# Kernel tuning notes

Measured on AMD Instinct MI355X. Metric: run time of the kernel, lower is better.

The kernel has to match this reference:

```python
import jax, jax.numpy as jnp
import numpy as np
from jax import lax

NH = 8        # num_heads
NWIN = 7      # n_win
TOPK = 4


def setup_inputs() -> dict:
    key = jax.random.key(0)
    ks = jax.random.split(key, 7)
    B, C, H, W = 16, 256, 56, 56
    x = jax.random.normal(ks[0], (B, C, H, W), dtype=jnp.float32)
    s = 1.0 / np.sqrt(C)
    qkv_w = jax.random.normal(ks[1], (3 * C, C), dtype=jnp.float32) * s   # 1x1 conv
    qkv_b = jnp.zeros((3 * C,), dtype=jnp.float32)
    lepe_w = jax.random.normal(ks[2], (C, 1, 5, 5), dtype=jnp.float32) * 0.2  # depthwise 5x5
    lepe_b = jnp.zeros((C,), dtype=jnp.float32)
    out_w = jax.random.normal(ks[3], (C, C), dtype=jnp.float32) * s       # 1x1 conv
    out_b = jnp.zeros((C,), dtype=jnp.float32)
    return {"x": x, "qkv_w": qkv_w, "qkv_b": qkv_b, "lepe_w": lepe_w,
            "lepe_b": lepe_b, "out_w": out_w, "out_b": out_b}


def reference(x, qkv_w, qkv_b, lepe_w, lepe_b, out_w, out_b):
    B, C, H, W = x.shape
    rs0, rs1 = max(1, H // NWIN), max(1, W // NWIN)   # region size (H,W assumed divisible)
    rh, rw = H // rs0, W // rs1
    nreg, reg = rh * rw, rs0 * rs1
    hd = C // NH
    scale = C ** (-0.5)

    # qkv projection (1x1 conv == channel matmul)
    qkv = jnp.einsum('bchw,oc->bohw', x, qkv_w) + qkv_b[None, :, None, None]
    q, k, v = jnp.split(qkv, 3, axis=1)

    # region-level pooling (avg_pool over exact region blocks)
    def pool(t):
        return t.reshape(B, C, rh, rs0, rw, rs1).mean(axis=(3, 5))  # (B,C,rh,rw)
    q_r = pool(q).reshape(B, C, nreg).transpose(0, 2, 1)   # (B, nreg, C)
    k_r = pool(k).reshape(B, C, nreg)                      # (B, C, nreg)
    a_r = q_r @ k_r                                        # (B, nreg, nreg)
    _, idx = lax.top_k(a_r, TOPK)                          # (B, nreg, topk)

    # grid -> sequence: (B,C,H,W) -> (B,NH,nreg,reg,hd)
    def g2s(t):
        t = t.reshape(B, NH, hd, rh, rs0, rw, rs1)
        t = t.transpose(0, 1, 3, 5, 4, 6, 2)  # b,m,h,w,p,q,d
        return t.reshape(B, NH, nreg, reg, hd)

    qs, ks_, vs = g2s(q), g2s(k), g2s(v)

    # gather top-k kv regions per query region
    idx_h = jnp.broadcast_to(idx[:, None], (B, NH, nreg, TOPK))
    gidx = idx_h.reshape(B, NH, nreg * TOPK)[..., None, None]   # (B,NH,nreg*topk,1,1)
    kg = jnp.take_along_axis(ks_, gidx, axis=2).reshape(B, NH, nreg, TOPK * reg, hd)
    vg = jnp.take_along_axis(vs, gidx, axis=2).reshape(B, NH, nreg, TOPK * reg, hd)

    attn = jax.nn.softmax(jnp.einsum('bhnrd,bhnkd->bhnrk', qs * scale, kg), axis=-1)
    out = jnp.einsum('bhnrk,bhnkd->bhnrd', attn, vg)  # (B,NH,nreg,reg,hd)

    # sequence -> grid
    out = out.reshape(B, NH, rh, rw, rs0, rs1, hd)
    out = out.transpose(0, 1, 6, 2, 4, 3, 5).reshape(B, C, H, W)

    # LePE: depthwise 5x5 conv on v
    lepe = lax.conv_general_dilated(v, lepe_w, (1, 1), 'SAME',
                                    feature_group_count=C,
                                    dimension_numbers=('NCHW', 'OIHW', 'NCHW'))
    lepe = lepe + lepe_b[None, :, None, None]

    out = out + lepe
    out = jnp.einsum('bchw,oc->bohw', out, out_w) + out_b[None, :, None, None]
    return out
```

## Files before the change

### kernel.cpp

```cpp
#include <hip/hip_runtime.h>

typedef __attribute__((ext_vector_type(8))) short short8;
typedef __attribute__((ext_vector_type(4))) float f32x4;
typedef unsigned int uint;

constexpr int Bn    = 16;
constexpr int Cn    = 256;
constexpr int Hn    = 56;
constexpr int Wn    = 56;
constexpr int HWn   = Hn * Wn;
constexpr int NPn   = 3200;
constexpr int NHn   = 8;
constexpr int RWn   = 7;
constexpr int NREGn = 49;
constexpr int TOPKn = 4;
constexpr float QKSf = 0.0625f * 1.44269504088896f;

__device__ __forceinline__ float b2f(ushort u) { return __builtin_bit_cast(float, (uint)u << 16); }
__device__ __forceinline__ float b2fl(uint u) { return __builtin_bit_cast(float, u << 16); }
__device__ __forceinline__ float b2fh(uint u) { return __builtin_bit_cast(float, u & 0xffff0000u); }
__device__ __forceinline__ ushort f2b(float f) {
    uint u = __builtin_bit_cast(uint, f);
    u = (u + 0x7fffu + ((u >> 16) & 1u)) >> 16;
    return (ushort)u;
}

typedef __attribute__((address_space(3))) uint lds_u32_t;
typedef __attribute__((address_space(1))) const uint glb_u32_t;
__device__ __forceinline__ void gl_lds16(const ushort* g, ushort* l) {
    __builtin_amdgcn_global_load_lds((glb_u32_t*)g, (lds_u32_t*)l, 16, 0, 0);
}

__global__ __launch_bounds__(256)
void fill_pads(uint* __restrict__ xt, uint* __restrict__ yt)
{
    const int gid = blockIdx.x * 256 + threadIdx.x;
    const int arr = gid >> 17;
    const int e   = gid & 131071;
    const int b   = e >> 13;
    const int off = e & 8191;
    uint* base = arr ? yt : xt;
    base[(size_t)b * (NPn * Cn / 2) + (HWn * Cn / 2) + off] = 0u;
}

__global__ __launch_bounds__(256)
void convert_w(const float* __restrict__ qw, const float* __restrict__ ow,
               ushort* __restrict__ wq, ushort* __restrict__ wo)
{
    const int e = (blockIdx.x * 256 + threadIdx.x) * 4;
    if (e < 196608) {
        const float4 v = *(const float4*)(qw + e);
        *(ushort4*)(wq + e) = make_ushort4(f2b(v.x), f2b(v.y), f2b(v.z), f2b(v.w));
    } else {
        const int e2 = e - 196608;
        const float4 v = *(const float4*)(ow + e2);
        *(ushort4*)(wo + e2) = make_ushort4(f2b(v.x), f2b(v.y), f2b(v.z), f2b(v.w));
    }
}

__global__ __launch_bounds__(256)
void convert_x(const float* __restrict__ x, ushort* __restrict__ xt)
{
    __shared__ float tile[64][65];
    const int p0 = blockIdx.x * 64, c0 = blockIdx.y * 64, b = blockIdx.z;
    const int tid = threadIdx.x;
    #pragma unroll
    for (int it = 0; it < 4; ++it) {
        const int slot = it * 256 + tid;
        const int c = slot >> 4, p4 = (slot & 15) << 2;
        const float4 v = *(const float4*)(x + ((size_t)b * Cn + c0 + c) * HWn + p0 + p4);
        tile[c][p4 + 0] = v.x; tile[c][p4 + 1] = v.y;
        tile[c][p4 + 2] = v.z; tile[c][p4 + 3] = v.w;
    }
    __syncthreads();
    #pragma unroll
    for (int it = 0; it < 4; ++it) {
        const int slot = it * 256 + tid;
        const int p = slot >> 4, c4 = (slot & 15) << 2;
        ushort4 w4 = make_ushort4(f2b(tile[c4 + 0][p]), f2b(tile[c4 + 1][p]),
                                  f2b(tile[c4 + 2][p]), f2b(tile[c4 + 3][p]));
        *(ushort4*)(xt + ((size_t)b * NPn + p0 + p) * Cn + c0 + c4) = w4;
    }
}

__global__ __launch_bounds__(256)
void pool_x(const float* __restrict__ x, float* __restrict__ xr)
{
    const int gid = blockIdx.x * 256 + threadIdx.x;
    if (gid >= Bn * Cn * NREGn) return;
    const int r = gid % NREGn;
    const int t = gid / NREGn;
    const int c = t % Cn, b = t / Cn;
    const float* plane = x + ((size_t)b * Cn + c) * HWn + (r / RWn) * 8 * Wn + (r % RWn) * 8;
    float s = 0.f;
    #pragma unroll
    for (int p = 0; p < 8; ++p) {
        const float4 a  = *(const float4*)(plane + p * Wn);
        const float4 b4 = *(const float4*)(plane + p * Wn + 4);
        s += a.x + a.y + a.z + a.w + b4.x + b4.y + b4.z + b4.w;
    }
    xr[gid] = s * (1.0f / 64.0f);
}

__global__ __launch_bounds__(256)
void qkr_gemm(const float* __restrict__ qw, const float* __restrict__ qb,
              const float* __restrict__ xr, float* __restrict__ qr,
              float* __restrict__ kr)
{
    const int gid = blockIdx.x * 256 + threadIdx.x;
    const int j = gid % NREGn;
    const int t = gid / NREGn;
    const int m = t & 511;
    const int b = t >> 9;
    const float* wr = qw + (size_t)m * Cn;
    const float* xb = xr + (size_t)b * Cn * NREGn + j;
    float s = 0.f;
    #pragma unroll 8
    for (int c = 0; c < Cn; ++c)
        s = fmaf(wr[c], xb[c * NREGn], s);
    s += qb[m];
    if (m < Cn) qr[((size_t)b * Cn + m) * NREGn + j] = s;
    else        kr[((size_t)b * Cn + (m - Cn)) * NREGn + j] = s;
}

__global__ __launch_bounds__(256)
void routing(const float* __restrict__ qr, const float* __restrict__ kr,
             int* __restrict__ idxo)
{
    const int ig = blockIdx.x, b = blockIdx.y;
    __shared__ float ksh[Cn][NREGn];
    __shared__ float qsh[Cn][7];
    __shared__ float ar[7][NREGn];
    const float* qb = qr + (size_t)b * Cn * NREGn;
    const float* kb = kr + (size_t)b * Cn * NREGn;
    for (int rr = 0; rr < NREGn; ++rr)
        ksh[threadIdx.x][rr] = kb[threadIdx.x * NREGn + rr];
    for (int e = threadIdx.x; e < Cn * 7; e += 256)
        qsh[e / 7][e % 7] = qb[(e / 7) * NREGn + ig * 7 + (e % 7)];
    __syncthreads();
    for (int e = threadIdx.x; e < 7 * NREGn; e += 256) {
        const int il = e / NREGn, j = e % NREGn;
        float s = 0.f;
        for (int c = 0; c < Cn; ++c)
            s = fmaf(qsh[c][il], ksh[c][j], s);
        ar[il][j] = s;
    }
    __syncthreads();
    if (threadIdx.x < 7) {
        const int il = threadIdx.x;
        float bv0 = -3.0e38f, bv1 = -3.0e38f, bv2 = -3.0e38f, bv3 = -3.0e38f;
        int bi0 = 0, bi1 = 0, bi2 = 0, bi3 = 0;
        for (int j = 0; j < NREGn; ++j) {
            const float v = ar[il][j];
            if (v > bv3) {
                if (v > bv0)      { bv3=bv2; bi3=bi2; bv2=bv1; bi2=bi1; bv1=bv0; bi1=bi0; bv0=v; bi0=j; }
                else if (v > bv1) { bv3=bv2; bi3=bi2; bv2=bv1; bi2=bi1; bv1=v; bi1=j; }
                else if (v > bv2) { bv3=bv2; bi3=bi2; bv2=v; bi2=j; }
                else              { bv3=v; bi3=j; }
            }
        }
        int* o = idxo + ((size_t)b * NREGn + ig * 7 + il) * TOPKn;
        o[0] = bi0; o[1] = bi1; o[2] = bi2; o[3] = bi3;
    }
}

template<int MODE>
__global__ __launch_bounds__(256)
void gemm_mfma(const ushort* __restrict__ Wb, const float* __restrict__ bias,
               const ushort* __restrict__ Bt,
               ushort* __restrict__ oq, ushort* __restrict__ ok,
               ushort* __restrict__ ovt, float* __restrict__ of)
{
    constexpr int K = Cn;
    int bb, bx, by;
    {
        const int flat = blockIdx.x;
        if (MODE == 0) {
            const int sw = (flat & 7) * 300 + (flat >> 3);
            bb = sw / 150; const int r2 = sw % 150; bx = r2 / 6; by = r2 % 6;
        } else {
            const int sw = (flat & 7) * 100 + (flat >> 3);
            bb = sw / 50;  const int r2 = sw % 50;  bx = r2 / 2; by = r2 % 2;
        }
    }
    const int n0 = bx * 128;
    const int m0 = by * 128;
    __shared__ ushort As[128 * 32];
    __shared__ ushort Bs[128 * 32];
    const int tid = threadIdx.x;
    const int wid = tid >> 6, lane = tid & 63;
    const int wm = wid >> 1, wn = wid & 1;
    const ushort* Bb = Bt + (size_t)bb * NPn * K;

    f32x4 acc[4][4];
    #pragma unroll
    for (int i = 0; i < 4; ++i)
        #pragma unroll
        for (int j = 0; j < 4; ++j)
            acc[i][j] = (f32x4){0.f, 0.f, 0.f, 0.f};

    const int cA = wid * 64 + lane;
    const int rowA = cA >> 2, koffA = (cA & 3) << 3;

    for (int k0 = 0; k0 < K; k0 += 32) {
        gl_lds16(Wb + (size_t)(m0 + rowA) * K + k0 + koffA, As + wid * 512);
        gl_lds16(Wb + (size_t)(m0 + rowA + 64) * K + k0 + koffA, As + 2048 + wid * 512);
        gl_lds16(Bb + (size_t)(n0 + rowA) * K + k0 + koffA, Bs + wid * 512);
        gl_lds16(Bb + (size_t)(n0 + rowA + 64) * K + k0 + koffA, Bs + 2048 + wid * 512);
        __syncthreads();
        short8 a[4], b[4];
        #pragma unroll
        for (int i = 0; i < 4; ++i)
            a[i] = *(const short8*)(As + (wm * 64 + i * 16 + (lane & 15)) * 32 + ((lane >> 4) << 3));
        #pragma unroll
        for (int j = 0; j < 4; ++j)
            b[j] = *(const short8*)(Bs + (wn * 64 + j * 16 + (lane & 15)) * 32 + ((lane >> 4) << 3));
        #pragma unroll
        for (int i = 0; i < 4; ++i)
            #pragma unroll
            for (int j = 0; j < 4; ++j)
                acc[i][j] = __builtin_amdgcn_mfma_f32_16x16x32_bf16(a[i], b[j], acc[i][j], 0, 0, 0);
        __syncthreads();
    }

    if (MODE == 0) {
        #pragma unroll
        for (int i = 0; i < 4; ++i) {
            const int m_base = m0 + wm * 64 + i * 16;
            const int which = m_base >> 8;
            const int hh = (m_base >> 5) & 7;
            const int db = (m_base & 31) + ((lane >> 4) << 2);
            const float4 b4 = *(const float4*)(bias + m_base + ((lane >> 4) << 2));
            #pragma unroll
            for (int j = 0; j < 4; ++j) {
                const int n = n0 + wn * 64 + j * 16 + (lane & 15);
                if (n < HWn) {
                    const int py = n / 56, px = n % 56;
                    const int rr = (py >> 3) * 7 + (px >> 3);
                    const int ss = ((py & 7) << 3) + (px & 7);
                    if (which == 0) {
                        ushort4 w4 = make_ushort4(
                            f2b((acc[i][j][0] + b4.x) * QKSf), f2b((acc[i][j][1] + b4.y) * QKSf),
                            f2b((acc[i][j][2] + b4.z) * QKSf), f2b((acc[i][j][3] + b4.w) * QKSf));
                        *(ushort4*)(oq + (((size_t)bb * NHn + hh) * HWn + rr * 64 + ss) * 32 + db) = w4;
                    } else if (which == 1) {
                        ushort4 w4 = make_ushort4(f2b(acc[i][j][0] + b4.x), f2b(acc[i][j][1] + b4.y),
                                                  f2b(acc[i][j][2] + b4.z), f2b(acc[i][j][3] + b4.w));
                        *(ushort4*)(ok + (((size_t)bb * NHn + hh) * HWn + rr * 64 + ss) * 32 + db) = w4;
                    } else {
                        const size_t vtb = ((size_t)(bb * NHn + hh) * 32 + db) * HWn + rr * 64 + ss;
                        ovt[vtb + 0 * HWn] = f2b(acc[i][j][0] + b4.x);
                        ovt[vtb + 1 * HWn] = f2b(acc[i][j][1] + b4.y);
                        ovt[vtb + 2 * HWn] = f2b(acc[i][j][2] + b4.z);
                        ovt[vtb + 3 * HWn] = f2b(acc[i][j][3] + b4.w);
                    }
                }
            }
        }
    } else {
        #pragma unroll
        for (int i = 0; i < 4; ++i) {
            const int mb = m0 + wm * 64 + i * 16 + ((lane >> 4) << 2);
            const float4 b4 = *(const float4*)(bias + mb);
            #pragma unroll
            for (int j = 0; j < 4; ++j) {
                const int n = n0 + wn * 64 + j * 16 + (lane & 15);
                if (n < HWn) {
                    const int rr = n >> 6, ss = n & 63;
                    const int py = (rr / 7) * 8 + (ss >> 3);
                    const int px = (rr % 7) * 8 + (ss & 7);
                    float* od = of + ((size_t)bb * Cn + mb) * HWn + py * 56 + px;
                    od[0 * HWn] = acc[i][j][0] + b4.x;
                    od[1 * HWn] = acc[i][j][1] + b4.y;
                    od[2 * HWn] = acc[i][j][2] + b4.z;
                    od[3 * HWn] = acc[i][j][3] + b4.w;
                }
            }
        }
    }
}

__global__ __launch_bounds__(256)
void lepe(const ushort* __restrict__ vt, const float* __restrict__ lw,
          const float* __restrict__ lb, ushort* __restrict__ lbuf)
{
    const int gid = blockIdx.x * 256 + threadIdx.x;
    const int plane = gid / 392;
    const int within = gid - plane * 392;
    const int row = within / 7;
    const int sx  = within - row * 7;
    const int px0 = sx * 8;
    const int c = plane & 255;
    const ushort* vp = vt + (size_t)plane * HWn;
    const float* wc = lw + c * 25;

    float wreg[25];
    #pragma unroll
    for (int i = 0; i < 25; ++i) wreg[i] = wc[i];

    float acc[8];
    const float bias = lb[c];
    #pragma unroll
    for (int j = 0; j < 8; ++j) acc[j] = bias;

    #pragma unroll
    for (int kh = 0; kh < 5; ++kh) {
        const int iy = row + kh - 2;
        if (iy < 0 || iy >= Hn) continue;
        const int ry = iy >> 3, il = iy & 7;
        const ushort* rp = vp + (ry * 7 + sx) * 64 + il * 8;
        const uint  a = *(const uint*)(rp - 64 + 6);
        const uint4 M = *(const uint4*)(rp);
        const uint  e = *(const uint*)(rp + 64);
        float w[12];
        w[0]  = (px0 >= 2)      ? b2fl(a)   : 0.f;
        w[1]  = (px0 >= 1)      ? b2fh(a)   : 0.f;
        w[2]  = b2fl(M.x); w[3]  = b2fh(M.x);
        w[4]  = b2fl(M.y); w[5]  = b2fh(M.y);
        w[6]  = b2fl(M.z); w[7]  = b2fh(M.z);
        w[8]  = b2fl(M.w); w[9]  = b2fh(M.w);
        w[10] = (px0 + 8 < Wn)  ? b2fl(e)   : 0.f;
        w[11] = (px0 + 9 < Wn)  ? b2fh(e)   : 0.f;
        #pragma unroll
        for (int kw = 0; kw < 5; ++kw) {
            const float ww = wreg[kh * 5 + kw];
            #pragma unroll
            for (int j = 0; j < 8; ++j)
                acc[j] = fmaf(w[j + kw], ww, acc[j]);
        }
    }
    ushort* op = lbuf + (size_t)plane * HWn + ((row >> 3) * 7 + sx) * 64 + (row & 7) * 8;
    *(ushort4*)(op)     = make_ushort4(f2b(acc[0]), f2b(acc[1]), f2b(acc[2]), f2b(acc[3]));
    *(ushort4*)(op + 4) = make_ushort4(f2b(acc[4]), f2b(acc[5]), f2b(acc[6]), f2b(acc[7]));
}

__global__ __launch_bounds__(256, 2)
void attention3(const ushort* __restrict__ qs, const ushort* __restrict__ ks,
                const ushort* __restrict__ vt, const int* __restrict__ idxp,
                const ushort* __restrict__ lep, ushort* __restrict__ yt)
{
    const int flat = blockIdx.x;
    const int sw = (flat & 7) * 196 + (flat >> 3);
    const int b = sw / 98;
    const int rem = sw % 98;
    const int r = rem % 49;
    const int wid = threadIdx.x >> 6, lane = threadIdx.x & 63;
    const int h = (rem / 49) * 4 + wid;
    const int col = lane & 15, g = lane >> 4;
    __shared__ ushort plds_all[4][4096];
    ushort* pw = plds_all[wid];

    const size_t hb = ((size_t)b * NHn + h) * HWn;
    const size_t vtb = (size_t)(b * NHn + h) * 32;

    short8 qf[4];
    #pragma unroll
    for (int qt = 0; qt < 4; ++qt)
        qf[qt] = *(const short8*)(qs + (hb + (size_t)r * 64 + qt * 16 + col) * 32 + g * 8);

    f32x4 o[4][2];
    #pragma unroll
    for (int qt = 0; qt < 4; ++qt) {
        o[qt][0] = (f32x4){0.f, 0.f, 0.f, 0.f};
        o[qt][1] = (f32x4){0.f, 0.f, 0.f, 0.f};
    }
    float mrow[4] = {-3.0e38f, -3.0e38f, -3.0e38f, -3.0e38f};
    float lrow[4] = {0.f, 0.f, 0.f, 0.f};

    const int* ip = idxp + ((size_t)b * NREGn + r) * TOPKn;

    for (int t = 0; t < TOPKn; ++t) {
        const int rr = ip[t];
        short8 kf[4];
        #pragma unroll
        for (int kt = 0; kt < 4; ++kt)
            kf[kt] = *(const short8*)(ks + (hb + (size_t)rr * 64 + kt * 16 + col) * 32 + g * 8);
        short8 vf[2][2];
        #pragma unroll
        for (int dt = 0; dt < 2; ++dt)
            #pragma unroll
            for (int kc = 0; kc < 2; ++kc)
                vf[dt][kc] = *(const short8*)(vt + (vtb + dt * 16 + col) * HWn
                                              + (size_t)rr * 64 + kc * 32 + g * 8);

        f32x4 s[4][4];
        #pragma unroll
        for (int qt = 0; qt < 4; ++qt)
            #pragma unroll
            for (int kt = 0; kt < 4; ++kt)
                s[qt][kt] = __builtin_amdgcn_mfma_f32_16x16x32_bf16(
                    kf[kt], qf[qt], (f32x4){0.f, 0.f, 0.f, 0.f}, 0, 0, 0);

        #pragma unroll
        for (int qt = 0; qt < 4; ++qt) {
            float mx = s[qt][0][0];
            #pragma unroll
            for (int kt = 0; kt < 4; ++kt)
                #pragma unroll
                for (int e = 0; e < 4; ++e)
                    mx = fmaxf(mx, s[qt][kt][e]);
            mx = fmaxf(mx, __shfl_xor(mx, 16));
            mx = fmaxf(mx, __shfl_xor(mx, 32));
            const float mnew = fmaxf(mrow[qt], mx);
            const float corr = exp2f(mrow[qt] - mnew);
            mrow[qt] = mnew;
            float ps = 0.f;
            #pragma unroll
            for (int kt = 0; kt < 4; ++kt)
                #pragma unroll
                for (int e = 0; e < 4; ++e) {
                    const float p = exp2f(s[qt][kt][e] - mnew);
                    s[qt][kt][e] = p; ps += p;
                }
            ps += __shfl_xor(ps, 16);
            ps += __shfl_xor(ps, 32);
            lrow[qt] = lrow[qt] * corr + ps;
            const int qrow = qt * 16 + col;
            const int swz = (qrow & 7) << 4;
            #pragma unroll
            for (int kt = 0; kt < 4; ++kt) {
                ushort4 pk = make_ushort4(f2b(s[qt][kt][0]), f2b(s[qt][kt][1]),
                                          f2b(s[qt][kt][2]), f2b(s[qt][kt][3]));
                const int byt = (qrow * 128 + kt * 32 + g * 8) ^ swz;
                *(ushort4*)((char*)pw + byt) = pk;
            }
            #pragma unroll
            for (int reg = 0; reg < 4; ++reg) {
                const float cr = __shfl(corr, g * 4 + reg);
                o[qt][0][reg] *= cr;
                o[qt][1][reg] *= cr;
            }
        }
        #pragma unroll
        for (int kc = 0; kc < 2; ++kc)
            #pragma unroll
            for (int qt = 0; qt < 4; ++qt) {
                const int qrow = qt * 16 + col;
                const int byt = (qrow * 128 + kc * 64 + g * 16) ^ ((qrow & 7) << 4);
                const short8 pf = *(const short8*)((const char*)pw + byt);
                o[qt][0] = __builtin_amdgcn_mfma_f32_16x16x32_bf16(pf, vf[0][kc], o[qt][0], 0, 0, 0);
                o[qt][1] = __builtin_amdgcn_mfma_f32_16x16x32_bf16(pf, vf[1][kc], o[qt][1], 0, 0, 0);
            }
    }

    #pragma unroll
    for (int qt = 0; qt < 4; ++qt) {
        const float linv = 1.0f / lrow[qt];
        #pragma unroll
        for (int reg = 0; reg < 4; ++reg) {
            const float li = __shfl(linv, g * 4 + reg);
            const int row = qt * 16 + g * 4 + reg;
            const int swz = ((row >> 1) & 3) << 4;
            #pragma unroll
            for (int dt = 0; dt < 2; ++dt) {
                const int byt = (row * 64 + (dt * 16 + col) * 2) ^ swz;
                *(ushort*)((char*)pw + byt) = f2b(o[qt][dt][reg] * li);
            }
        }
    }
    const ushort* lp = lep + ((size_t)b * Cn + h * 32) * HWn + (size_t)r * 64 + lane;
    ushort* yp = yt + ((size_t)b * NPn + (size_t)r * 64 + lane) * Cn + h * 32;
    const int swl = ((lane >> 1) & 3) << 4;
    #pragma unroll
    for (int c4 = 0; c4 < 8; ++c4) {
        const int byt = (lane * 64 + c4 * 8) ^ swl;
        const ushort4 ov = *(const ushort4*)((const char*)pw + byt);
        ushort4 w4 = make_ushort4(
            f2b(b2f(ov.x) + b2f(lp[(size_t)(c4 * 4 + 0) * HWn])),
            f2b(b2f(ov.y) + b2f(lp[(size_t)(c4 * 4 + 1) * HWn])),
            f2b(b2f(ov.z) + b2f(lp[(size_t)(c4 * 4 + 2) * HWn])),
            f2b(b2f(ov.w) + b2f(lp[(size_t)(c4 * 4 + 3) * HWn])));
        *(ushort4*)(yp + c4 * 4) = w4;
    }
}

extern "C" void kernel_launch(void* const* d_in, const int* in_sizes, int n_in,
                              void* d_out, int out_size, void* d_ws, size_t ws_size,
                              hipStream_t stream)
{
    const float* x      = (const float*)d_in[0];
    const float* qkv_w  = (const float*)d_in[1];
    const float* qkv_b  = (const float*)d_in[2];
    const float* lepe_w = (const float*)d_in[3];
    const float* lepe_b = (const float*)d_in[4];
    const float* out_w  = (const float*)d_in[5];
    const float* out_b  = (const float*)d_in[6];
    float* out = (float*)d_out;

    char* ws = (char*)d_ws;
    ushort* XT = (ushort*)(ws);
    ushort* YT = (ushort*)(ws + 26214400);
    ushort* QS = (ushort*)(ws + 52428800);
    ushort* KS = (ushort*)(ws + 78118912);
    ushort* VT = (ushort*)(ws + 103809024);
    ushort* LB = (ushort*)(ws + 129499136);
    ushort* WQ = (ushort*)(ws + 155189248);
    ushort* WO = (ushort*)(ws + 155582464);
    float*  XR = (float*)(ws + 155713536);
    float*  QR = (float*)(ws + 156516352);
    float*  KR = (float*)(ws + 157319168);
    int*   IDX = (int*)(ws + 158121984);

    fill_pads<<<1024, 256, 0, stream>>>((uint*)XT, (uint*)YT);
    convert_w<<<256, 256, 0, stream>>>(qkv_w, out_w, WQ, WO);
    convert_x<<<dim3(49, 4, 16), 256, 0, stream>>>(x, XT);
    pool_x<<<(Bn * Cn * NREGn + 255) / 256, 256, 0, stream>>>(x, XR);
    qkr_gemm<<<1568, 256, 0, stream>>>(qkv_w, qkv_b, XR, QR, KR);
    routing<<<dim3(7, 16), 256, 0, stream>>>(QR, KR, IDX);
    gemm_mfma<0><<<2400, 256, 0, stream>>>(WQ, qkv_b, XT, QS, KS, VT, nullptr);
    lepe<<<6272, 256, 0, stream>>>(VT, lepe_w, lepe_b, LB);
    attention3<<<1568, 256, 0, stream>>>(QS, KS, VT, IDX, LB, YT);
    gemm_mfma<1><<<800, 256, 0, stream>>>(WO, out_b, YT, nullptr, nullptr, nullptr, out);
}
```

Before: 258.4 us.

## Use hardware bf16 pack, prefetch KV tiles, lazy softmax rescale, drop pad fill

Replaces the software round-to-nearest bf16 conversion with the packed v_cvt_pk_bf16_f32 instruction in every kernel. The attention kernel now double-buffers K/V fragments for the next top-k region and interleaves the score MFMAs per query tile. It also skips the online-softmax max/rescale update unless the running max grows by more than 8. Other changes: the fill_pads kernel is removed (padding rows in XT/YT are no longer zeroed), and the routing K load is coalesced. The lazy rescale and the missing pad zeroing could alter numerics if the GEMM reads uninitialized pad rows.

```diff
diff --git a/kernel.cpp b/kernel.cpp
--- a/kernel.cpp
+++ b/kernel.cpp
@@ -19,10 +19,10 @@
 __device__ __forceinline__ float b2f(ushort u) { return __builtin_bit_cast(float, (uint)u << 16); }
 __device__ __forceinline__ float b2fl(uint u) { return __builtin_bit_cast(float, u << 16); }
 __device__ __forceinline__ float b2fh(uint u) { return __builtin_bit_cast(float, u & 0xffff0000u); }
-__device__ __forceinline__ ushort f2b(float f) {
-    uint u = __builtin_bit_cast(uint, f);
-    u = (u + 0x7fffu + ((u >> 16) & 1u)) >> 16;
-    return (ushort)u;
+__device__ __forceinline__ uint cvtpk(float lo, float hi) {
+    uint r;
+    asm("v_cvt_pk_bf16_f32 %0, %1, %2" : "=v"(r) : "v"(lo), "v"(hi));
+    return r;
 }
 
 typedef __attribute__((address_space(3))) uint lds_u32_t;
@@ -32,29 +32,19 @@
 }
 
 __global__ __launch_bounds__(256)
-void fill_pads(uint* __restrict__ xt, uint* __restrict__ yt)
-{
-    const int gid = blockIdx.x * 256 + threadIdx.x;
-    const int arr = gid >> 17;
-    const int e   = gid & 131071;
-    const int b   = e >> 13;
-    const int off = e & 8191;
-    uint* base = arr ? yt : xt;
-    base[(size_t)b * (NPn * Cn / 2) + (HWn * Cn / 2) + off] = 0u;
-}
-
-__global__ __launch_bounds__(256)
 void convert_w(const float* __restrict__ qw, const float* __restrict__ ow,
                ushort* __restrict__ wq, ushort* __restrict__ wo)
 {
     const int e = (blockIdx.x * 256 + threadIdx.x) * 4;
     if (e < 196608) {
         const float4 v = *(const float4*)(qw + e);
-        *(ushort4*)(wq + e) = make_ushort4(f2b(v.x), f2b(v.y), f2b(v.z), f2b(v.w));
+        uint2 w; w.x = cvtpk(v.x, v.y); w.y = cvtpk(v.z, v.w);
+        *(uint2*)(wq + e) = w;
     } else {
         const int e2 = e - 196608;
         const float4 v = *(const float4*)(ow + e2);
-        *(ushort4*)(wo + e2) = make_ushort4(f2b(v.x), f2b(v.y), f2b(v.z), f2b(v.w));
+        uint2 w; w.x = cvtpk(v.x, v.y); w.y = cvtpk(v.z, v.w);
+        *(uint2*)(wo + e2) = w;
     }
 }
 
@@ -77,9 +67,10 @@
     for (int it = 0; it < 4; ++it) {
         const int slot = it * 256 + tid;
         const int p = slot >> 4, c4 = (slot & 15) << 2;
-        ushort4 w4 = make_ushort4(f2b(tile[c4 + 0][p]), f2b(tile[c4 + 1][p]),
-                                  f2b(tile[c4 + 2][p]), f2b(tile[c4 + 3][p]));
-        *(ushort4*)(xt + ((size_t)b * NPn + p0 + p) * Cn + c0 + c4) = w4;
+        uint2 w;
+        w.x = cvtpk(tile[c4 + 0][p], tile[c4 + 1][p]);
+        w.y = cvtpk(tile[c4 + 2][p], tile[c4 + 3][p]);
+        *(uint2*)(xt + ((size_t)b * NPn + p0 + p) * Cn + c0 + c4) = w;
     }
 }
 
@@ -133,8 +124,8 @@
     __shared__ float ar[7][NREGn];
     const float* qb = qr + (size_t)b * Cn * NREGn;
     const float* kb = kr + (size_t)b * Cn * NREGn;
-    for (int rr = 0; rr < NREGn; ++rr)
-        ksh[threadIdx.x][rr] = kb[threadIdx.x * NREGn + rr];
+    for (int e = threadIdx.x; e < Cn * NREGn; e += 256)
+        ksh[e / NREGn][e % NREGn] = kb[e];
     for (int e = threadIdx.x; e < Cn * 7; e += 256)
         qsh[e / 7][e % 7] = qb[(e / 7) * NREGn + ig * 7 + (e % 7)];
     __syncthreads();
@@ -239,20 +230,23 @@
                     const int rr = (py >> 3) * 7 + (px >> 3);
                     const int ss = ((py & 7) << 3) + (px & 7);
                     if (which == 0) {
-                        ushort4 w4 = make_ushort4(
-                            f2b((acc[i][j][0] + b4.x) * QKSf), f2b((acc[i][j][1] + b4.y) * QKSf),
-                            f2b((acc[i][j][2] + b4.z) * QKSf), f2b((acc[i][j][3] + b4.w) * QKSf));
-                        *(ushort4*)(oq + (((size_t)bb * NHn + hh) * HWn + rr * 64 + ss) * 32 + db) = w4;
+                        uint2 w;
+                        w.x = cvtpk((acc[i][j][0] + b4.x) * QKSf, (acc[i][j][1] + b4.y) * QKSf);
+                        w.y = cvtpk((acc[i][j][2] + b4.z) * QKSf, (acc[i][j][3] + b4.w) * QKSf);
+                        *(uint2*)(oq + (((size_t)bb * NHn + hh) * HWn + rr * 64 + ss) * 32 + db) = w;
                     } else if (which == 1) {
-                        ushort4 w4 = make_ushort4(f2b(acc[i][j][0] + b4.x), f2b(acc[i][j][1] + b4.y),
-                                                  f2b(acc[i][j][2] + b4.z), f2b(acc[i][j][3] + b4.w));
-                        *(ushort4*)(ok + (((size_t)bb * NHn + hh) * HWn + rr * 64 + ss) * 32 + db) = w4;
+                        uint2 w;
+                        w.x = cvtpk(acc[i][j][0] + b4.x, acc[i][j][1] + b4.y);
+                        w.y = cvtpk(acc[i][j][2] + b4.z, acc[i][j][3] + b4.w);
+                        *(uint2*)(ok + (((size_t)bb * NHn + hh) * HWn + rr * 64 + ss) * 32 + db) = w;
                     } else {
                         const size_t vtb = ((size_t)(bb * NHn + hh) * 32 + db) * HWn + rr * 64 + ss;
-                        ovt[vtb + 0 * HWn] = f2b(acc[i][j][0] + b4.x);
-                        ovt[vtb + 1 * HWn] = f2b(acc[i][j][1] + b4.y);
-                        ovt[vtb + 2 * HWn] = f2b(acc[i][j][2] + b4.z);
-                        ovt[vtb + 3 * HWn] = f2b(acc[i][j][3] + b4.w);
+                        const uint lo = cvtpk(acc[i][j][0] + b4.x, acc[i][j][1] + b4.y);
+                        const uint hi = cvtpk(acc[i][j][2] + b4.z, acc[i][j][3] + b4.w);
+                        ovt[vtb + 0 * HWn] = (ushort)lo;
+                        ovt[vtb + 1 * HWn] = (ushort)(lo >> 16);
+                        ovt[vtb + 2 * HWn] = (ushort)hi;
+                        ovt[vtb + 3 * HWn] = (ushort)(hi >> 16);
                     }
                 }
             }
@@ -330,8 +324,11 @@
         }
     }
     ushort* op = lbuf + (size_t)plane * HWn + ((row >> 3) * 7 + sx) * 64 + (row & 7) * 8;
-    *(ushort4*)(op)     = make_ushort4(f2b(acc[0]), f2b(acc[1]), f2b(acc[2]), f2b(acc[3]));
-    *(ushort4*)(op + 4) = make_ushort4(f2b(acc[4]), f2b(acc[5]), f2b(acc[6]), f2b(acc[7]));
+    uint2 wa, wb;
+    wa.x = cvtpk(acc[0], acc[1]); wa.y = cvtpk(acc[2], acc[3]);
+    wb.x = cvtpk(acc[4], acc[5]); wb.y = cvtpk(acc[6], acc[7]);
+    *(uint2*)(op)     = wa;
+    *(uint2*)(op + 4) = wb;
 }
 
 __global__ __launch_bounds__(256, 2)
@@ -368,69 +365,90 @@
     float lrow[4] = {0.f, 0.f, 0.f, 0.f};
 
     const int* ip = idxp + ((size_t)b * NREGn + r) * TOPKn;
-
+    const int4 i4 = *(const int4*)ip;
+    const int idxs[4] = {i4.x, i4.y, i4.z, i4.w};
+
+    short8 kfA[4], vfA[4];
+    {
+        const int rr = idxs[0];
+        #pragma unroll
+        for (int kt = 0; kt < 4; ++kt)
+            kfA[kt] = *(const short8*)(ks + (hb + (size_t)rr * 64 + kt * 16 + col) * 32 + g * 8);
+        #pragma unroll
+        for (int dt = 0; dt < 2; ++dt)
+            #pragma unroll
+            for (int kc = 0; kc < 2; ++kc)
+                vfA[dt * 2 + kc] = *(const short8*)(vt + (vtb + dt * 16 + col) * HWn
+                                                    + (size_t)rr * 64 + kc * 32 + g * 8);
+    }
+
+    #pragma unroll
     for (int t = 0; t < TOPKn; ++t) {
-        const int rr = ip[t];
-        short8 kf[4];
-        #pragma unroll
-        for (int kt = 0; kt < 4; ++kt)
-            kf[kt] = *(const short8*)(ks + (hb + (size_t)rr * 64 + kt * 16 + col) * 32 + g * 8);
-        short8 vf[2][2];
-        #pragma unroll
-        for (int dt = 0; dt < 2; ++dt)
-            #pragma unroll
-            for (int kc = 0; kc < 2; ++kc)
-                vf[dt][kc] = *(const short8*)(vt + (vtb + dt * 16 + col) * HWn
-                                              + (size_t)rr * 64 + kc * 32 + g * 8);
-
-        f32x4 s[4][4];
-        #pragma unroll
-        for (int qt = 0; qt < 4; ++qt)
+        short8 kfB[4], vfB[4];
+        if (t < 3) {
+            const int rr = idxs[t + 1];
             #pragma unroll
             for (int kt = 0; kt < 4; ++kt)
-                s[qt][kt] = __builtin_amdgcn_mfma_f32_16x16x32_bf16(
-                    kf[kt], qf[qt], (f32x4){0.f, 0.f, 0.f, 0.f}, 0, 0, 0);
+                kfB[kt] = *(const short8*)(ks + (hb + (size_t)rr * 64 + kt * 16 + col) * 32 + g * 8);
+            #pragma unroll
+            for (int dt = 0; dt < 2; ++dt)
+                #pragma unroll
+                for (int kc = 0; kc < 2; ++kc)
+                    vfB[dt * 2 + kc] = *(const short8*)(vt + (vtb + dt * 16 + col) * HWn
+                                                         + (size_t)rr * 64 + kc * 32 + g * 8);
+        }
 
         #pragma unroll
         for (int qt = 0; qt < 4; ++qt) {
-            float mx = s[qt][0][0];
+            f32x4 s[4];
+            #pragma unroll
+            for (int kt = 0; kt < 4; ++kt)
+                s[kt] = __builtin_amdgcn_mfma_f32_16x16x32_bf16(
+                    kfA[kt], qf[qt], (f32x4){0.f, 0.f, 0.f, 0.f}, 0, 0, 0);
+
+            float mx = s[0][0];
             #pragma unroll
             for (int kt = 0; kt < 4; ++kt)
                 #pragma unroll
                 for (int e = 0; e < 4; ++e)
-                    mx = fmaxf(mx, s[qt][kt][e]);
+                    mx = fmaxf(mx, s[kt][e]);
             mx = fmaxf(mx, __shfl_xor(mx, 16));
             mx = fmaxf(mx, __shfl_xor(mx, 32));
-            const float mnew = fmaxf(mrow[qt], mx);
-            const float corr = exp2f(mrow[qt] - mnew);
-            mrow[qt] = mnew;
+            if (!__all(mx - mrow[qt] <= 8.f)) {
+                const float mnew = fmaxf(mrow[qt], mx);
+                const float corr = exp2f(mrow[qt] - mnew);
+                mrow[qt] = mnew;
+                lrow[qt] *= corr;
+                #pragma unroll
+                for (int reg = 0; reg < 4; ++reg) {
+                    const float cr = __shfl(corr, g * 4 + reg);
+                    o[qt][0][reg] *= cr;
+                    o[qt][1][reg] *= cr;
+                }
+            }
             float ps = 0.f;
             #pragma unroll
             for (int kt = 0; kt < 4; ++kt)
                 #pragma unroll
                 for (int e = 0; e < 4; ++e) {
-                    const float p = exp2f(s[qt][kt][e] - mnew);
-                    s[qt][kt][e] = p; ps += p;
+                    const float p = exp2f(s[kt][e] - mrow[qt]);
+                    s[kt][e] = p; ps += p;
                 }
             ps += __shfl_xor(ps, 16);
             ps += __shfl_xor(ps, 32);
-            lrow[qt] = lrow[qt] * corr + ps;
+            lrow[qt] += ps;
             const int qrow = qt * 16 + col;
             const int swz = (qrow & 7) << 4;
             #pragma unroll
             for (int kt = 0; kt < 4; ++kt) {
-                ushort4 pk = make_ushort4(f2b(s[qt][kt][0]), f2b(s[qt][kt][1]),
-                                          f2b(s[qt][kt][2]), f2b(s[qt][kt][3]));
+                uint2 pk;
+                pk.x = cvtpk(s[kt][0], s[kt][1]);
+                pk.y = cvtpk(s[kt][2], s[kt][3]);
                 const int byt = (qrow * 128 + kt * 32 + g * 8) ^ swz;
-                *(ushort4*)((char*)pw + byt) = pk;
+                *(uint2*)((char*)pw + byt) = pk;
             }
-            #pragma unroll
-            for (int reg = 0; reg < 4; ++reg) {
-                const float cr = __shfl(corr, g * 4 + reg);
-                o[qt][0][reg] *= cr;
-                o[qt][1][reg] *= cr;
-            }
-        }
+        }
+
         #pragma unroll
         for (int kc = 0; kc < 2; ++kc)
             #pragma unroll
@@ -438,9 +456,14 @@
                 const int qrow = qt * 16 + col;
                 const int byt = (qrow * 128 + kc * 64 + g * 16) ^ ((qrow & 7) << 4);
                 const short8 pf = *(const short8*)((const char*)pw + byt);
-                o[qt][0] = __builtin_amdgcn_mfma_f32_16x16x32_bf16(pf, vf[0][kc], o[qt][0], 0, 0, 0);
-                o[qt][1] = __builtin_amdgcn_mfma_f32_16x16x32_bf16(pf, vf[1][kc], o[qt][1], 0, 0, 0);
+                o[qt][0] = __builtin_amdgcn_mfma_f32_16x16x32_bf16(pf, vfA[0 * 2 + kc], o[qt][0], 0, 0, 0);
+                o[qt][1] = __builtin_amdgcn_mfma_f32_16x16x32_bf16(pf, vfA[1 * 2 + kc], o[qt][1], 0, 0, 0);
             }
+
+        if (t < 3) {
+            #pragma unroll
+            for (int i = 0; i < 4; ++i) { kfA[i] = kfB[i]; vfA[i] = vfB[i]; }
+        }
     }
 
     #pragma unroll
@@ -451,11 +474,11 @@
             const float li = __shfl(linv, g * 4 + reg);
             const int row = qt * 16 + g * 4 + reg;
             const int swz = ((row >> 1) & 3) << 4;
-            #pragma unroll
-            for (int dt = 0; dt < 2; ++dt) {
-                const int byt = (row * 64 + (dt * 16 + col) * 2) ^ swz;
-                *(ushort*)((char*)pw + byt) = f2b(o[qt][dt][reg] * li);
-            }
+            const uint pk = cvtpk(o[qt][0][reg] * li, o[qt][1][reg] * li);
+            const int byt0 = (row * 64 + col * 2) ^ swz;
+            const int byt1 = (row * 64 + (16 + col) * 2) ^ swz;
+            *(ushort*)((char*)pw + byt0) = (ushort)pk;
+            *(ushort*)((char*)pw + byt1) = (ushort)(pk >> 16);
         }
     }
     const ushort* lp = lep + ((size_t)b * Cn + h * 32) * HWn + (size_t)r * 64 + lane;
@@ -465,12 +488,12 @@
     for (int c4 = 0; c4 < 8; ++c4) {
         const int byt = (lane * 64 + c4 * 8) ^ swl;
         const ushort4 ov = *(const ushort4*)((const char*)pw + byt);
-        ushort4 w4 = make_ushort4(
-            f2b(b2f(ov.x) + b2f(lp[(size_t)(c4 * 4 + 0) * HWn])),
-            f2b(b2f(ov.y) + b2f(lp[(size_t)(c4 * 4 + 1) * HWn])),
-            f2b(b2f(ov.z) + b2f(lp[(size_t)(c4 * 4 + 2) * HWn])),
-            f2b(b2f(ov.w) + b2f(lp[(size_t)(c4 * 4 + 3) * HWn])));
-        *(ushort4*)(yp + c4 * 4) = w4;
+        const float a0 = b2f(ov.x) + b2f(lp[(size_t)(c4 * 4 + 0) * HWn]);
+        const float a1 = b2f(ov.y) + b2f(lp[(size_t)(c4 * 4 + 1) * HWn]);
+        const float a2 = b2f(ov.z) + b2f(lp[(size_t)(c4 * 4 + 2) * HWn]);
+        const float a3 = b2f(ov.w) + b2f(lp[(size_t)(c4 * 4 + 3) * HWn]);
+        uint2 w4; w4.x = cvtpk(a0, a1); w4.y = cvtpk(a2, a3);
+        *(uint2*)(yp + c4 * 4) = w4;
     }
 }
 
@@ -501,7 +524,6 @@
     float*  KR = (float*)(ws + 157319168);
     int*   IDX = (int*)(ws + 158121984);
 
-    fill_pads<<<1024, 256, 0, stream>>>((uint*)XT, (uint*)YT);
     convert_w<<<256, 256, 0, stream>>>(qkv_w, out_w, WQ, WO);
     convert_x<<<dim3(49, 4, 16), 256, 0, stream>>>(x, XT);
     pool_x<<<(Bn * Cn * NREGn + 255) / 256, 256, 0, stream>>>(x, XR);
```

Result: faster. 243.5 us (-5.8%).
